# Optimization experiments

Measured on AMD Instinct MI355X. Metric: run time of the kernel, lower is better.

## Reference

```python
import jax, jax.numpy as jnp
import numpy as np

B, T, C = 2, 2048, 1024
H = 16
HD = C // H  # head_size = 64
FF = 2 * C   # ffwd_size default = n_embd * 2
EPS = float(jnp.finfo(jnp.float32).eps)  # torch RMSNorm eps=None -> finfo eps


def rmsnorm(x, g):
    # torch.nn.RMSNorm: x / sqrt(mean(x^2) + eps) * weight
    ms = jnp.mean(jnp.square(x), axis=-1, keepdims=True)
    return x * jax.lax.rsqrt(ms + EPS) * g


def setup_inputs() -> dict:
    key = jax.random.key(0)
    ks = jax.random.split(key, 12)
    s_in = 1.0 / np.sqrt(C)
    s_ff = 1.0 / np.sqrt(FF)
    return {
        "target": jax.random.normal(ks[0], (B, T, C), dtype=jnp.float32),
        # per-head projections, torch Linear layout [out, in] stacked over heads: [H, HD, C]
        "wq": jax.random.uniform(ks[1], (H, HD, C), jnp.float32, -s_in, s_in),
        "wk": jax.random.uniform(ks[2], (H, HD, C), jnp.float32, -s_in, s_in),
        "wv": jax.random.uniform(ks[3], (H, HD, C), jnp.float32, -s_in, s_in),
        "w_proj": jax.random.uniform(ks[4], (C, H * HD), jnp.float32, -s_in, s_in),
        "b_proj": jax.random.uniform(ks[5], (C,), jnp.float32, -s_in, s_in),
        "w1": jax.random.uniform(ks[6], (FF, C), jnp.float32, -s_in, s_in),
        "b1": jax.random.uniform(ks[7], (FF,), jnp.float32, -s_in, s_in),
        "w2": jax.random.uniform(ks[8], (C, FF), jnp.float32, -s_ff, s_ff),
        "b2": jax.random.uniform(ks[9], (C,), jnp.float32, -s_ff, s_ff),
        "g1": jnp.ones((C,), jnp.float32),
        "g2": jnp.ones((C,), jnp.float32),
    }


def reference(target, wq, wk, wv, w_proj, b_proj, w1, b1, w2, b2, g1, g2):
    x = rmsnorm(target, g1)
    # q,k,v: [B,H,T,HD]
    q = jnp.einsum("btc,hdc->bhtd", x, wq)
    k = jnp.einsum("btc,hdc->bhtd", x, wk)
    v = jnp.einsum("btc,hdc->bhtd", x, wv)
    scale = HD ** -0.5
    wei = jnp.einsum("bhtd,bhsd->bhts", q, k) * scale  # [B,H,T,T]
    causal = jnp.tril(jnp.ones((T, T), dtype=bool))
    wei = jnp.where(causal, wei, -jnp.inf)
    wei = jax.nn.softmax(wei, axis=-1)
    attn = jnp.einsum("bhts,bhsd->bhtd", wei, v)  # [B,H,T,HD]
    attn = attn.transpose(0, 2, 1, 3).reshape(B, T, H * HD)  # concat heads
    attn = attn @ w_proj.T + b_proj
    target = target + attn
    y = rmsnorm(target, g2)
    h = jax.nn.gelu(y @ w1.T + b1, approximate=False)  # torch nn.GELU default = exact
    ff = h @ w2.T + b2
    return target + ff
```

## Files before the change

### kernel.cpp

```cpp
#include <hip/hip_runtime.h>
#include <math.h>

#define B_  2
#define T_  2048
#define C_  1024
#define H_  16
#define HD_ 64
#define FF_ 2048
#define EPS_ 1.1920929e-07f

typedef __attribute__((ext_vector_type(8))) short short8;
typedef __attribute__((ext_vector_type(4))) float f32x4;
typedef __attribute__((ext_vector_type(16))) float f32x16;
typedef __attribute__((ext_vector_type(2))) __bf16 bf16x2v;
typedef __attribute__((ext_vector_type(4))) unsigned uint4v;

__device__ __forceinline__ unsigned short f2bf(float f) {
    unsigned u = __float_as_uint(f);
    u += 0x7fffu + ((u >> 16) & 1u);
    return (unsigned short)(u >> 16);
}
__device__ __forceinline__ float bf2f(unsigned short u) {
    return __uint_as_float(((unsigned)u) << 16);
}
__device__ __forceinline__ unsigned pk2bf(float a, float b) {
    bf16x2v v;
    v[0] = (__bf16)a;
    v[1] = (__bf16)b;
    return __builtin_bit_cast(unsigned, v);
}

__global__ void prep_kernel(const float* __restrict__ wq, const float* __restrict__ wk,
                            const float* __restrict__ wv, const float* __restrict__ wp,
                            const float* __restrict__ w1, const float* __restrict__ w2,
                            unsigned short* __restrict__ wb,
                            const float* __restrict__ x, const float* __restrict__ g,
                            unsigned short* __restrict__ y) {
    int tid = threadIdx.x;
    if (blockIdx.x < 8192) {
        size_t i = ((size_t)blockIdx.x * 256 + tid) * 4;
        const float* src; size_t off = i;
        if      (i < 1048576u)  { src = wq; }
        else if (i < 2097152u)  { src = wk; off = i - 1048576u; }
        else if (i < 3145728u)  { src = wv; off = i - 2097152u; }
        else if (i < 4194304u)  { src = wp; off = i - 3145728u; }
        else if (i < 6291456u)  { src = w1; off = i - 4194304u; }
        else                    { src = w2; off = i - 6291456u; }
        float4 v4 = *(const float4*)(src + off);
        ushort4 o4;
        o4.x = f2bf(v4.x); o4.y = f2bf(v4.y); o4.z = f2bf(v4.z); o4.w = f2bf(v4.w);
        *(ushort4*)(wb + i) = o4;
    } else {
        int row = blockIdx.x - 8192;
        const float4* xr = (const float4*)(x + (size_t)row * C_);
        float4 xv = xr[tid];
        float ss = xv.x * xv.x + xv.y * xv.y + xv.z * xv.z + xv.w * xv.w;
        #pragma unroll
        for (int m = 32; m >= 1; m >>= 1) ss += __shfl_xor(ss, m, 64);
        __shared__ float sred[4];
        if ((tid & 63) == 0) sred[tid >> 6] = ss;
        __syncthreads();
        float tot = sred[0] + sred[1] + sred[2] + sred[3];
        float r = rsqrtf(tot * (1.0f / C_) + EPS_);
        float4 gv = ((const float4*)g)[tid];
        ushort4 o;
        o.x = f2bf(xv.x * r * gv.x);
        o.y = f2bf(xv.y * r * gv.y);
        o.z = f2bf(xv.z * r * gv.z);
        o.w = f2bf(xv.w * r * gv.w);
        *((ushort4*)(y + (size_t)row * C_) + tid) = o;
    }
}

__global__ void rmsnorm_bf16_kernel(const float* __restrict__ x, const float* __restrict__ g,
                                    unsigned short* __restrict__ y) {
    int row = blockIdx.x;
    int tid = threadIdx.x;
    const float4* xr = (const float4*)(x + (size_t)row * C_);
    float4 xv = xr[tid];
    float ss = xv.x * xv.x + xv.y * xv.y + xv.z * xv.z + xv.w * xv.w;
    #pragma unroll
    for (int m = 32; m >= 1; m >>= 1) ss += __shfl_xor(ss, m, 64);
    __shared__ float sred[4];
    if ((tid & 63) == 0) sred[tid >> 6] = ss;
    __syncthreads();
    float tot = sred[0] + sred[1] + sred[2] + sred[3];
    float r = rsqrtf(tot * (1.0f / C_) + EPS_);
    float4 gv = ((const float4*)g)[tid];
    ushort4 o;
    o.x = f2bf(xv.x * r * gv.x);
    o.y = f2bf(xv.y * r * gv.y);
    o.z = f2bf(xv.z * r * gv.z);
    o.w = f2bf(xv.w * r * gv.w);
    *((ushort4*)(y + (size_t)row * C_) + tid) = o;
}

template <int TM, int ACT, bool BIAS, bool RES, bool OBF16, int ROUTE>
__global__ __launch_bounds__(256) void mfma_gemm(
        const unsigned short* __restrict__ A, const unsigned short* __restrict__ W,
        const float* __restrict__ bias, const float* __restrict__ resid,
        void* __restrict__ O0, void* __restrict__ O1, void* __restrict__ O2,
        int M, int N, int K) {
    constexpr int ACH = TM / 8;
    constexpr int NCH = (ACH + 16) / 4;
    constexpr int MI  = TM / 32;
    __shared__ short As[2 * TM * 32];
    __shared__ short Bs[2 * 128 * 32];
    const int tid  = threadIdx.x;
    const int w    = tid >> 6, lane = tid & 63;
    const int tileN = blockIdx.x * 128, tileM = blockIdx.y * TM;

    const unsigned short* gsrc[NCH];
    short* ldst[NCH];
    #pragma unroll
    for (int i2 = 0; i2 < NCH; ++i2) {
        int c = w * NCH + i2;
        if (c < ACH) {
            int kh = c / (ACH / 2), lc = c % (ACH / 2);
            gsrc[i2] = A + (size_t)(tileM + lc * 16 + (lane >> 2)) * K + kh * 32 + (lane & 3) * 8;
            ldst[i2] = As + c * 512;
        } else {
            int c2 = c - ACH;
            int kh = c2 >> 3, lc = c2 & 7;
            gsrc[i2] = W + (size_t)(tileN + lc * 16 + (lane >> 2)) * K + kh * 32 + (lane & 3) * 8;
            ldst[i2] = Bs + c2 * 512;
        }
    }

    f32x4 acc[MI][4];
    const f32x4 zed = {0.f, 0.f, 0.f, 0.f};
    #pragma unroll
    for (int i = 0; i < MI; ++i)
        #pragma unroll
        for (int j = 0; j < 4; ++j) acc[i][j] = zed;

    const int wm = (w >> 1) * (TM / 2), wn = (w & 1) * 64;
    const int frow = lane & 15, koff = (lane >> 4) * 8;

    for (int k0 = 0; k0 < K; k0 += 64) {
        #pragma unroll
        for (int i2 = 0; i2 < NCH; ++i2)
            __builtin_amdgcn_global_load_lds(
                (const __attribute__((address_space(1))) unsigned*)(gsrc[i2] + k0),
                (__attribute__((address_space(3))) unsigned*)ldst[i2], 16, 0, 0);
        __syncthreads();

        #pragma unroll
        for (int kh = 0; kh < 2; ++kh) {
            short8 af[MI], bfr[4];
            #pragma unroll
            for (int i = 0; i < MI; ++i)
                af[i] = *(const short8*)(As + kh * TM * 32 + (wm + i * 16 + frow) * 32 + koff);
            #pragma unroll
            for (int j = 0; j < 4; ++j)
                bfr[j] = *(const short8*)(Bs + kh * 128 * 32 + (wn + j * 16 + frow) * 32 + koff);
            #pragma unroll
            for (int i = 0; i < MI; ++i)
                #pragma unroll
                for (int j = 0; j < 4; ++j)
                    acc[i][j] = __builtin_amdgcn_mfma_f32_16x16x32_bf16(af[i], bfr[j], acc[i][j], 0, 0, 0);
        }
        __syncthreads();
    }

    const int ecol = lane & 15, erow = (lane >> 4) * 4;
    const int zone = ROUTE ? (tileN >> 10) : 0;
    #pragma unroll
    for (int j = 0; j < 4; ++j) {
        int n = tileN + wn + j * 16 + ecol;
        float bv = BIAS ? bias[n] : 0.f;
        int nl = ROUTE ? (n & 1023) : n;
        #pragma unroll
        for (int i = 0; i < MI; ++i) {
            int mbase = tileM + wm + i * 16 + erow;
            #pragma unroll
            for (int r = 0; r < 4; ++r) {
                float val = acc[i][j][r] + bv;
                if (ACT == 1) val = 0.5f * val * (1.0f + erff(val * 0.70710678118654752f));
                int mrow = mbase + r;
                if (ROUTE) {
                    if (zone == 0) {
                        ((unsigned short*)O0)[(size_t)mrow * 1024 + nl] = f2bf(val * 0.18033688011112042f);
                    } else if (zone == 1) {
                        ((unsigned short*)O1)[(size_t)mrow * 1024 + nl] = f2bf(val);
                    } else {
                        int bb = mrow >> 11, tt = mrow & 2047;
                        int hh = nl >> 6, dd = nl & 63;
                        ((unsigned short*)O2)[((size_t)((bb * 16 + hh) * 64 + dd)) * 2048 + tt] = f2bf(val);
                    }
                } else {
                    size_t idx = (size_t)mrow * N + n;
                    if (RES) val += resid[idx];
                    if (OBF16) ((unsigned short*)O0)[idx] = f2bf(val);
                    else       ((float*)O0)[idx] = val;
                }
            }
        }
    }
}

__global__ __launch_bounds__(256, 3) void flash_mfma_kernel(
        const unsigned short* __restrict__ q, const unsigned short* __restrict__ k,
        const unsigned short* __restrict__ vT, unsigned short* __restrict__ out) {
    __shared__ unsigned short KsA[64 * 64];
    __shared__ unsigned short VtA[64 * 64];
    __shared__ unsigned short KsB[64 * 64];
    __shared__ unsigned short VtB[64 * 64];

    const int tid  = threadIdx.x;
    const int w    = tid >> 6, lane = tid & 63;
    const int l31  = lane & 31, hi = lane >> 5;
    const int bh   = blockIdx.x;
    const int qt   = (gridDim.y - 1) - blockIdx.y;
    const int h = bh & (H_ - 1);
    const int b = bh >> 4;

    const size_t qkbase = (size_t)b * T_ * C_ + h * HD_;
    const size_t vbase  = (size_t)(b * H_ + h) * HD_ * T_;

    const int wq = qt * 128 + w * 32;
    const int qg = wq + l31;

    short8 QB[4];
    {
        const unsigned short* qp = q + qkbase + (size_t)qg * C_ + hi * 8;
        QB[0] = *(const short8*)(qp);
        QB[1] = *(const short8*)(qp + 16);
        QB[2] = *(const short8*)(qp + 32);
        QB[3] = *(const short8*)(qp + 48);
    }

    f32x16 O0, O1;
    #pragma unroll
    for (int i = 0; i < 16; ++i) { O0[i] = 0.f; O1[i] = 0.f; }
    float l_i = 0.f;

    const int r8 = lane >> 3, c7 = lane & 7;
    const int cswz = (c7 ^ r8) * 8;
    const int rxA = l31 & 7;

    auto stageKV = [&](unsigned short* Ksb, unsigned short* Vtb, int tt) {
        const int s0_ = tt * 64;
        #pragma unroll
        for (int c = 0; c < 2; ++c) {
            const int row = w * 16 + c * 8 + r8;
            const unsigned short* gk = k + qkbase + (size_t)(s0_ + row) * C_ + cswz;
            __builtin_amdgcn_global_load_lds(
                (const __attribute__((address_space(1))) unsigned*)gk,
                (__attribute__((address_space(3))) unsigned*)(Ksb + (w * 16 + c * 8) * 64), 16, 0, 0);
            const unsigned short* gv = vT + vbase + (size_t)row * T_ + s0_ + cswz;
            __builtin_amdgcn_global_load_lds(
                (const __attribute__((address_space(1))) unsigned*)gv,
                (__attribute__((address_space(3))) unsigned*)(Vtb + (w * 16 + c * 8) * 64), 16, 0, 0);
        }
    };

    auto computeTile = [&](const unsigned short* Ksb, const unsigned short* Vtb, int tt) {
        const int s0 = tt * 64;
        if (s0 > wq + 31) return;
        const bool diag = (s0 + 63 > wq);

        f32x16 S0, S1;
        #pragma unroll
        for (int i = 0; i < 16; ++i) { S0[i] = 0.f; S1[i] = 0.f; }
        {
            const unsigned short* kr0 = Ksb + l31 * 64;
            const unsigned short* kr1 = Ksb + (32 + l31) * 64;
            #pragma unroll
            for (int ks = 0; ks < 4; ++ks) {
                short8 KA0 = *(const short8*)(kr0 + (((ks << 1) | hi) ^ rxA) * 8);
                short8 KA1 = *(const short8*)(kr1 + (((ks << 1) | hi) ^ rxA) * 8);
                S0 = __builtin_amdgcn_mfma_f32_32x32x16_bf16(KA0, QB[ks], S0, 0, 0, 0);
                S1 = __builtin_amdgcn_mfma_f32_32x32x16_bf16(KA1, QB[ks], S1, 0, 0, 0);
            }
        }

        float rs = 0.f;
        #pragma unroll
        for (int r = 0; r < 16; ++r) {
            float e0 = __builtin_amdgcn_exp2f(S0[r]);
            float e1 = __builtin_amdgcn_exp2f(S1[r]);
            if (diag) {
                int sg = s0 + (r & 3) + 8 * (r >> 2) + 4 * hi;
                e0 = (sg > qg) ? 0.f : e0;
                e1 = (sg + 32 > qg) ? 0.f : e1;
            }
            S0[r] = e0; S1[r] = e1;
            rs += e0 + e1;
        }
        rs += __shfl_xor(rs, 32, 64);
        l_i += rs;

        short8 PA[4];
        #pragma unroll
        for (int sb = 0; sb < 2; ++sb) {
            float p0  = sb ? S1[0]  : S0[0],  p1  = sb ? S1[1]  : S0[1];
            float p2  = sb ? S1[2]  : S0[2],  p3  = sb ? S1[3]  : S0[3];
            float p4  = sb ? S1[4]  : S0[4],  p5  = sb ? S1[5]  : S0[5];
            float p6  = sb ? S1[6]  : S0[6],  p7  = sb ? S1[7]  : S0[7];
            float p8  = sb ? S1[8]  : S0[8],  p9  = sb ? S1[9]  : S0[9];
            float p10 = sb ? S1[10] : S0[10], p11 = sb ? S1[11] : S0[11];
            float p12 = sb ? S1[12] : S0[12], p13 = sb ? S1[13] : S0[13];
            float p14 = sb ? S1[14] : S0[14], p15 = sb ? S1[15] : S0[15];
            unsigned xw0 = pk2bf(p0,  p1),  xw1 = pk2bf(p2,  p3);
            unsigned yw0 = pk2bf(p4,  p5),  yw1 = pk2bf(p6,  p7);
            unsigned xw2 = pk2bf(p8,  p9),  xw3 = pk2bf(p10, p11);
            unsigned yw2 = pk2bf(p12, p13), yw3 = pk2bf(p14, p15);
            unsigned xs0 = (unsigned)__shfl_xor((int)xw0, 32, 64);
            unsigned ys0 = (unsigned)__shfl_xor((int)yw0, 32, 64);
            unsigned xs1 = (unsigned)__shfl_xor((int)xw1, 32, 64);
            unsigned ys1 = (unsigned)__shfl_xor((int)yw1, 32, 64);
            unsigned xs2 = (unsigned)__shfl_xor((int)xw2, 32, 64);
            unsigned ys2 = (unsigned)__shfl_xor((int)yw2, 32, 64);
            unsigned xs3 = (unsigned)__shfl_xor((int)xw3, 32, 64);
            unsigned ys3 = (unsigned)__shfl_xor((int)yw3, 32, 64);
            uint4v w0, w1;
            w0[0] = hi ? ys0 : xw0;
            w0[1] = hi ? ys1 : xw1;
            w0[2] = hi ? yw0 : xs0;
            w0[3] = hi ? yw1 : xs1;
            w1[0] = hi ? ys2 : xw2;
            w1[1] = hi ? ys3 : xw3;
            w1[2] = hi ? yw2 : xs2;
            w1[3] = hi ? yw3 : xs3;
            PA[sb * 2 + 0] = __builtin_bit_cast(short8, w0);
            PA[sb * 2 + 1] = __builtin_bit_cast(short8, w1);
        }

        __builtin_amdgcn_s_setprio(1);
        {
            const unsigned short* vr0 = Vtb + l31 * 64;
            const unsigned short* vr1 = Vtb + (32 + l31) * 64;
            #pragma unroll
            for (int ks = 0; ks < 4; ++ks) {
                short8 VB0 = *(const short8*)(vr0 + (((ks << 1) | hi) ^ rxA) * 8);
                short8 VB1 = *(const short8*)(vr1 + (((ks << 1) | hi) ^ rxA) * 8);
                O0 = __builtin_amdgcn_mfma_f32_32x32x16_bf16(PA[ks], VB0, O0, 0, 0, 0);
                O1 = __builtin_amdgcn_mfma_f32_32x32x16_bf16(PA[ks], VB1, O1, 0, 0, 0);
            }
        }
        __builtin_amdgcn_s_setprio(0);
    };

    const int NT = 2 * qt + 2;
    stageKV(KsA, VtA, 0);
    __syncthreads();
    int tt = 0;
    for (;;) {
        if (tt + 1 < NT) stageKV(KsB, VtB, tt + 1);
        computeTile(KsA, VtA, tt);
        __syncthreads();
        ++tt; if (tt >= NT) break;
        if (tt + 1 < NT) stageKV(KsA, VtA, tt + 1);
        computeTile(KsB, VtB, tt);
        __syncthreads();
        ++tt; if (tt >= NT) break;
    }

    float inv = 1.0f / l_i;
    #pragma unroll
    for (int r = 0; r < 16; ++r) {
        int ql = (r & 3) + 8 * (r >> 2) + 4 * hi;
        float invr = __shfl(inv, ql, 64);
        int row = wq + ql;
        size_t obase = ((size_t)(b * T_ + row)) * C_ + h * HD_ + l31;
        out[obase]      = f2bf(O0[r] * invr);
        out[obase + 32] = f2bf(O1[r] * invr);
    }
}

extern "C" void kernel_launch(void* const* d_in, const int* in_sizes, int n_in,
                              void* d_out, int out_size, void* d_ws, size_t ws_size,
                              hipStream_t stream) {
    const float* target = (const float*)d_in[0];
    const float* wq     = (const float*)d_in[1];
    const float* wk     = (const float*)d_in[2];
    const float* wv     = (const float*)d_in[3];
    const float* w_proj = (const float*)d_in[4];
    const float* b_proj = (const float*)d_in[5];
    const float* w1     = (const float*)d_in[6];
    const float* b1     = (const float*)d_in[7];
    const float* w2     = (const float*)d_in[8];
    const float* b2     = (const float*)d_in[9];
    const float* g1     = (const float*)d_in[10];
    const float* g2     = (const float*)d_in[11];
    float* out = (float*)d_out;

    char* ws = (char*)d_ws;
    const size_t MB = 1u << 20;
    unsigned short* xn = (unsigned short*)(ws);
    unsigned short* q  = (unsigned short*)(ws + 8 * MB);
    unsigned short* k  = (unsigned short*)(ws + 16 * MB);
    unsigned short* vt = (unsigned short*)(ws + 24 * MB);
    float*          x2 = (float*)(ws + 32 * MB);
    unsigned short* wb = (unsigned short*)(ws + 48 * MB);
    unsigned short* y  = q;
    unsigned short* hb = k;

    unsigned short* wqkv_b = wb;
    unsigned short* wp_b   = wb + 3145728u;
    unsigned short* w1_b   = wb + 4194304u;
    unsigned short* w2_b   = wb + 6291456u;

    const int M = B_ * T_;

    prep_kernel<<<12288, 256, 0, stream>>>(wq, wk, wv, w_proj, w1, w2, wb, target, g1, xn);

    mfma_gemm<128, 0, false, false, true, 1><<<dim3(24, M / 128), 256, 0, stream>>>(
        xn, wqkv_b, nullptr, nullptr, q, k, vt, M, 3072, C_);

    flash_mfma_kernel<<<dim3(B_ * H_, T_ / 128), 256, 0, stream>>>(q, k, vt, xn);

    mfma_gemm<64, 0, true, true, false, 0><<<dim3(C_ / 128, M / 64), 256, 0, stream>>>(
        xn, wp_b, b_proj, target, x2, nullptr, nullptr, M, C_, C_);

    rmsnorm_bf16_kernel<<<M, 256, 0, stream>>>(x2, g2, y);

    mfma_gemm<64, 1, true, false, true, 0><<<dim3(FF_ / 128, M / 64), 256, 0, stream>>>(
        y, w1_b, b1, nullptr, hb, nullptr, nullptr, M, FF_, C_);

    mfma_gemm<64, 0, true, true, false, 0><<<dim3(C_ / 128, M / 64), 256, 0, stream>>>(
        hb, w2_b, b2, x2, out, nullptr, nullptr, M, C_, FF_);
}
```

Baseline: 287.2 us.

## Split flash attention KV range across wave pairs and swizzle GEMM tile order

```diff
diff --git a/kernel.cpp b/kernel.cpp
--- a/kernel.cpp
+++ b/kernel.cpp
@@ -108,7 +108,12 @@
     __shared__ short Bs[2 * 128 * 32];
     const int tid  = threadIdx.x;
     const int w    = tid >> 6, lane = tid & 63;
-    const int tileN = blockIdx.x * 128, tileM = blockIdx.y * TM;
+
+    const int gx  = gridDim.x;
+    const int nwg = gx * gridDim.y;
+    const int wg  = blockIdx.y * gx + blockIdx.x;
+    const int swz = (wg & 7) * (nwg >> 3) + (wg >> 3);
+    const int tileN = (swz % gx) * 128, tileM = (swz / gx) * TM;
 
     const unsigned short* gsrc[NCH];
     short* ldst[NCH];
@@ -199,7 +204,7 @@
     }
 }
 
-__global__ __launch_bounds__(256, 3) void flash_mfma_kernel(
+__global__ __launch_bounds__(256, 4) void flash_mfma_kernel(
         const unsigned short* __restrict__ q, const unsigned short* __restrict__ k,
         const unsigned short* __restrict__ vT, unsigned short* __restrict__ out) {
     __shared__ unsigned short KsA[64 * 64];
@@ -210,6 +215,7 @@
     const int tid  = threadIdx.x;
     const int w    = tid >> 6, lane = tid & 63;
     const int l31  = lane & 31, hi = lane >> 5;
+    const int qh   = w & 1, kvp = w >> 1;
     const int bh   = blockIdx.x;
     const int qt   = (gridDim.y - 1) - blockIdx.y;
     const int h = bh & (H_ - 1);
@@ -218,8 +224,8 @@
     const size_t qkbase = (size_t)b * T_ * C_ + h * HD_;
     const size_t vbase  = (size_t)(b * H_ + h) * HD_ * T_;
 
-    const int wq = qt * 128 + w * 32;
-    const int qg = wq + l31;
+    const int wqv = qt * 64 + qh * 32;
+    const int qg  = wqv + l31;
 
     short8 QB[4];
     {
@@ -257,8 +263,7 @@
 
     auto computeTile = [&](const unsigned short* Ksb, const unsigned short* Vtb, int tt) {
         const int s0 = tt * 64;
-        if (s0 > wq + 31) return;
-        const bool diag = (s0 + 63 > wq);
+        const bool diag = (s0 + 63 > wqv);
 
         f32x16 S0, S1;
         #pragma unroll
@@ -342,30 +347,59 @@
         __builtin_amdgcn_s_setprio(0);
     };
 
-    const int NT = 2 * qt + 2;
+    const int NT = qt + 1;
     stageKV(KsA, VtA, 0);
     __syncthreads();
     int tt = 0;
     for (;;) {
         if (tt + 1 < NT) stageKV(KsB, VtB, tt + 1);
-        computeTile(KsA, VtA, tt);
+        if ((tt & 1) == kvp) computeTile(KsA, VtA, tt);
         __syncthreads();
         ++tt; if (tt >= NT) break;
         if (tt + 1 < NT) stageKV(KsA, VtA, tt + 1);
-        computeTile(KsB, VtB, tt);
+        if ((tt & 1) == kvp) computeTile(KsB, VtB, tt);
         __syncthreads();
         ++tt; if (tt >= NT) break;
     }
 
-    float inv = 1.0f / l_i;
-    #pragma unroll
-    for (int r = 0; r < 16; ++r) {
-        int ql = (r & 3) + 8 * (r >> 2) + 4 * hi;
-        float invr = __shfl(inv, ql, 64);
-        int row = wq + ql;
-        size_t obase = ((size_t)(b * T_ + row)) * C_ + h * HD_ + l31;
-        out[obase]      = f2bf(O0[r] * invr);
-        out[obase + 32] = f2bf(O1[r] * invr);
+    float* Of = (float*)(qh ? KsB : KsA);
+    float* lF = (float*)VtA;
+    if (kvp == 1) {
+        #pragma unroll
+        for (int i4 = 0; i4 < 4; ++i4) {
+            f32x4 a, c;
+            a[0] = O0[i4 * 4 + 0]; a[1] = O0[i4 * 4 + 1];
+            a[2] = O0[i4 * 4 + 2]; a[3] = O0[i4 * 4 + 3];
+            c[0] = O1[i4 * 4 + 0]; c[1] = O1[i4 * 4 + 1];
+            c[2] = O1[i4 * 4 + 2]; c[3] = O1[i4 * 4 + 3];
+            *(f32x4*)(Of + (i4 * 64 + lane) * 4)       = a;
+            *(f32x4*)(Of + ((4 + i4) * 64 + lane) * 4) = c;
+        }
+        if (lane < 32) lF[qh * 32 + l31] = l_i;
+    }
+    __syncthreads();
+    if (kvp == 0) {
+        #pragma unroll
+        for (int i4 = 0; i4 < 4; ++i4) {
+            f32x4 a = *(const f32x4*)(Of + (i4 * 64 + lane) * 4);
+            f32x4 c = *(const f32x4*)(Of + ((4 + i4) * 64 + lane) * 4);
+            O0[i4 * 4 + 0] += a[0]; O0[i4 * 4 + 1] += a[1];
+            O0[i4 * 4 + 2] += a[2]; O0[i4 * 4 + 3] += a[3];
+            O1[i4 * 4 + 0] += c[0]; O1[i4 * 4 + 1] += c[1];
+            O1[i4 * 4 + 2] += c[2]; O1[i4 * 4 + 3] += c[3];
+        }
+        l_i += lF[qh * 32 + l31];
+
+        float inv = 1.0f / l_i;
+        #pragma unroll
+        for (int r = 0; r < 16; ++r) {
+            int ql = (r & 3) + 8 * (r >> 2) + 4 * hi;
+            float invr = __shfl(inv, ql, 64);
+            int row = wqv + ql;
+            size_t obase = ((size_t)(b * T_ + row)) * C_ + h * HD_ + l31;
+            out[obase]      = f2bf(O0[r] * invr);
+            out[obase + 32] = f2bf(O1[r] * invr);
+        }
     }
 }
 
@@ -409,7 +443,7 @@
     mfma_gemm<128, 0, false, false, true, 1><<<dim3(24, M / 128), 256, 0, stream>>>(
         xn, wqkv_b, nullptr, nullptr, q, k, vt, M, 3072, C_);
 
-    flash_mfma_kernel<<<dim3(B_ * H_, T_ / 128), 256, 0, stream>>>(q, k, vt, xn);
+    flash_mfma_kernel<<<dim3(B_ * H_, T_ / 64), 256, 0, stream>>>(q, k, vt, xn);
 
     mfma_gemm<64, 0, true, true, false, 0><<<dim3(C_ / 128, M / 64), 256, 0, stream>>>(
         xn, wp_b, b_proj, target, x2, nullptr, nullptr, M, C_, C_);
```

After: 289.8 us. About the same (+0.9%).
